# Kernel optimization log

Hardware: AMD Instinct MI355X
Metric: run time of the kernel (lower is better)

## Reference

```python
import jax, jax.numpy as jnp
import numpy as np

T, D, H, E, K = 4096, 1024, 2048, 8, 2  # tokens, model dim, expert hidden, n_experts, top_k
AUX_COEF = 0.01


def setup_inputs() -> dict:
    key = jax.random.key(0)
    ks = jax.random.split(key, 8)
    sd = lambda fan_in: 1.0 / np.sqrt(fan_in)
    x = jax.random.normal(ks[0], (T, D), jnp.float32)
    Wr = jax.random.normal(ks[1], (E, D), jnp.float32) * sd(D)      # router (no bias)
    w1 = jax.random.normal(ks[2], (E, H, D), jnp.float32) * sd(D)   # stacked up-proj
    w2 = jax.random.normal(ks[3], (E, D, H), jnp.float32) * sd(H)   # stacked down-proj
    w3 = jax.random.normal(ks[4], (E, H, D), jnp.float32) * sd(D)   # stacked gate-proj
    w1s = jax.random.normal(ks[5], (H, D), jnp.float32) * sd(D)     # shared expert
    w2s = jax.random.normal(ks[6], (D, H), jnp.float32) * sd(H)
    w3s = jax.random.normal(ks[7], (H, D), jnp.float32) * sd(D)
    return dict(x=x, Wr=Wr, w1=w1, w2=w2, w3=w3, w1s=w1s, w2s=w2s, w3s=w3s)


def _gelu(v):
    return jax.nn.gelu(v, approximate=False)  # torch F.gelu default = exact erf


def reference(x, Wr, w1, w2, w3, w1s, w2s, w3s):
    n_tok = x.shape[0]
    router_out = x @ Wr.T                                   # [T, E]
    router_probs = jax.nn.softmax(router_out, axis=-1)
    _, topk_idx = jax.lax.top_k(router_out, K)              # [T, K]
    topk_probs, _ = jax.lax.top_k(router_probs, K)          # top-k of probs (same order)

    # auxiliary load-balance loss (first-choice density * mean prob)
    expert_mask = jax.nn.one_hot(topk_idx[:, 0], E, dtype=jnp.float32)
    density = expert_mask.mean(axis=0)
    aux_loss = AUX_COEF * jnp.sum(density * router_probs.mean(axis=0)) * E

    # combine weights C[t, e] = sum of routed probs for expert e at token t
    C = jnp.zeros((n_tok, E), x.dtype).at[
        jnp.arange(n_tok)[:, None], topk_idx
    ].add(topk_probs)

    # dense per-expert SwiGLU-style FFN, combined by C (equal math to
    # sort-based dispatch + scatter_add in the original)
    h = _gelu(jnp.einsum('td,ehd->teh', x, w1)) * jnp.einsum('td,ehd->teh', x, w3)
    ye = jnp.einsum('teh,edh->ted', h, w2)                  # [T, E, D]
    out = jnp.einsum('ted,te->td', ye, C)

    # shared expert (always active)
    out = out + (_gelu(x @ w1s.T) * (x @ w3s.T)) @ w2s.T
    return out, aux_loss
```

## Files before the change

### kernel.cpp

```cpp
#include <hip/hip_runtime.h>
#include <hip/hip_bf16.h>
#include <cstdint>

#define T_TOK 4096
#define DMODEL 1024
#define HDIM 2048

typedef short bf16x8 __attribute__((ext_vector_type(8)));
typedef float f32x4 __attribute__((ext_vector_type(4)));
typedef uint32_t u32x4 __attribute__((ext_vector_type(4)));

__device__ __forceinline__ uint32_t cvt_pk_bf16(float lo, float hi) {
  uint32_t d;
  asm("v_cvt_pk_bf16_f32 %0, %1, %2" : "=v"(d) : "v"(lo), "v"(hi));
  return d;
}
__device__ __forceinline__ unsigned short f2bf(float f) {
  uint32_t d;
  asm("v_cvt_pk_bf16_f32 %0, %1, %1" : "=v"(d) : "v"(f));
  return (unsigned short)d;
}
__device__ __forceinline__ float gelu_erf(float v) {
  return 0.5f * v * (1.0f + erff(v * 0.70710678118654752f));
}
__device__ __forceinline__ void gload16(const void* g, void* lds) {
  __builtin_amdgcn_global_load_lds((const __attribute__((address_space(1))) void*)g,
                                   (__attribute__((address_space(3))) void*)lds, 16, 0, 0);
}
__device__ __forceinline__ u32x4 pk8(const float* s) {
  float4 v0 = ((const float4*)s)[0], v1 = ((const float4*)s)[1];
  u32x4 p = {cvt_pk_bf16(v0.x, v0.y), cvt_pk_bf16(v0.z, v0.w),
             cvt_pk_bf16(v1.x, v1.y), cvt_pk_bf16(v1.z, v1.w)};
  return p;
}

__global__ __launch_bounds__(256) void convert_w(
    const float* __restrict__ w1, const float* __restrict__ w3,
    const float* __restrict__ w1s, const float* __restrict__ w3s,
    const float* __restrict__ w2, const float* __restrict__ w2s,
    short* __restrict__ wu, short* __restrict__ wg, short* __restrict__ wd) {
  int bid = blockIdx.x;
  if (bid < 9216) {
    int id = bid * 256 + threadIdx.x;
    int e = id >> 18, rem = id & 262143;
    int h16 = rem >> 11, d32 = (rem >> 6) & 31, ln = rem & 63;
    size_t so = (size_t)(h16 * 16 + (ln & 15)) * DMODEL + d32 * 32 + (ln >> 4) * 8;
    const float* s1 = (e < 8) ? w1 + (size_t)e * 2097152 + so : w1s + so;
    const float* s3 = (e < 8) ? w3 + (size_t)e * 2097152 + so : w3s + so;
    *(u32x4*)(wu + (size_t)id * 8) = pk8(s1);
    *(u32x4*)(wg + (size_t)id * 8) = pk8(s3);
  } else {
    int id = (bid - 9216) * 256 + threadIdx.x;
    int e = id >> 18, rem = id & 262143;
    int d16 = rem >> 12, h32 = (rem >> 6) & 63, ln = rem & 63;
    size_t so = (size_t)(d16 * 16 + (ln & 15)) * HDIM + h32 * 32 + (ln >> 4) * 8;
    const float* s2 = (e < 8) ? w2 + (size_t)e * 2097152 + so : w2s + so;
    *(u32x4*)(wd + (size_t)id * 8) = pk8(s2);
  }
}

__global__ __launch_bounds__(256) void router_kernel(
    const float* __restrict__ x, const float* __restrict__ Wr,
    int* __restrict__ cursor, int* __restrict__ cnt1,
    float* __restrict__ psum, int* __restrict__ perm, float* __restrict__ pw,
    short* __restrict__ xb) {
  __shared__ float4 sW[8 * 256];
  __shared__ float sP[8];
  int tid = threadIdx.x;
  const float4* W4 = (const float4*)Wr;
  for (int i = tid; i < 2048; i += 256) sW[i] = W4[i];
  if (tid < 8) sP[tid] = 0.f;
  __syncthreads();

  int lane = tid & 63, wid = tid >> 6;
  int t = blockIdx.x * 4 + wid;
  float acc[8] = {0.f, 0.f, 0.f, 0.f, 0.f, 0.f, 0.f, 0.f};
  const float4* x4 = (const float4*)(x + (size_t)t * DMODEL);
#pragma unroll
  for (int it = 0; it < 4; ++it) {
    float4 xv = x4[it * 64 + lane];
    uint2 pk = {cvt_pk_bf16(xv.x, xv.y), cvt_pk_bf16(xv.z, xv.w)};
    *(uint2*)(xb + (size_t)t * DMODEL + it * 256 + lane * 4) = pk;
#pragma unroll
    for (int e = 0; e < 8; ++e) {
      float4 wv = sW[e * 256 + it * 64 + lane];
      acc[e] += xv.x * wv.x + xv.y * wv.y + xv.z * wv.z + xv.w * wv.w;
    }
  }
#pragma unroll
  for (int e = 0; e < 8; ++e)
    for (int off = 32; off; off >>= 1) acc[e] += __shfl_xor(acc[e], off);

  float mx = acc[0];
#pragma unroll
  for (int e = 1; e < 8; ++e) mx = fmaxf(mx, acc[e]);
  float ex[8], s = 0.f;
#pragma unroll
  for (int e = 0; e < 8; ++e) { ex[e] = expf(acc[e] - mx); s += ex[e]; }
  float inv = 1.f / s;
  int e0 = 0;
#pragma unroll
  for (int e = 1; e < 8; ++e) if (acc[e] > acc[e0]) e0 = e;
  int e1 = (e0 == 0) ? 1 : 0;
#pragma unroll
  for (int e = 0; e < 8; ++e) if (e != e0 && acc[e] > acc[e1]) e1 = e;

  if (lane == 0) {
#pragma unroll
    for (int e = 0; e < 8; ++e) atomicAdd(&sP[e], ex[e] * inv);
    atomicAdd(&cnt1[e0], 1);
    int s0 = atomicAdd(&cursor[e0], 1);
    perm[e0 * 4096 + s0] = t; pw[e0 * 4096 + s0] = ex[e0] * inv;
    int s1 = atomicAdd(&cursor[e1], 1);
    perm[e1 * 4096 + s1] = t; pw[e1 * 4096 + s1] = ex[e1] * inv;
  }
  __syncthreads();
  if (tid < 8) atomicAdd(&psum[tid], sP[tid]);
}

__global__ void finalize_kernel(const int* __restrict__ cursor,
                                const int* __restrict__ cnt1,
                                const float* __restrict__ psum,
                                int* __restrict__ base, float* __restrict__ aux_out) {
  if (threadIdx.x == 0) {
    int b = 0;
    for (int e = 0; e < 8; ++e) { base[e] = b; b += ((cursor[e] + 127) >> 7) << 7; }
    base[8] = b;
    float aux = 0.f;
    for (int e = 0; e < 8; ++e)
      aux += ((float)cnt1[e] * (1.f / T_TOK)) * (psum[e] * (1.f / T_TOK));
    aux_out[0] = 0.01f * 8.f * aux;
  }
}

__global__ __launch_bounds__(256, 2) void gemm_upgate(
    const short* __restrict__ xb,
    const short* __restrict__ wu, const short* __restrict__ wg,
    const int* __restrict__ cursor, const int* __restrict__ base,
    const int* __restrict__ perm, unsigned short* __restrict__ hbuf) {
  int e = blockIdx.z, mt = blockIdx.y, nt = blockIdx.x;
  int cnt = (e < 8) ? cursor[e] : 4096;
  if (mt * 128 >= cnt) return;
  int hb = base[e];
  const short* wuE = wu + (size_t)e * 2097152;
  const short* wgE = wg + (size_t)e * 2097152;

  __shared__ short As[2][4096], Bs1[2][4096], Bs3[2][4096];

  int tid = threadIdx.x, lane = tid & 63, wid = tid >> 6;
  int fr = lane & 15, ko8 = (lane >> 4) * 8;
  int wr = wid >> 1, wc = wid & 1;

  size_t aOff[2], bOff[2];
#pragma unroll
  for (int s = 0; s < 2; ++s) {
    int g = s * 4 + wid;
    int slot = mt * 128 + g * 16 + fr;
    int tok = (e == 8) ? slot : ((slot < cnt) ? perm[e * 4096 + slot] : 0);
    aOff[s] = (size_t)tok * DMODEL + ko8;
    bOff[s] = ((size_t)(nt * 8 + g) * 32 * 64 + lane) * 8;
  }

  f32x4 acc1[4][4] = {}, acc3[4][4] = {};

  auto stage = [&](int buf, int it) {
#pragma unroll
    for (int s = 0; s < 2; ++s) {
      int g = s * 4 + wid;
      gload16(xb + aOff[s] + it * 32, &As[buf][g * 512 + lane * 8]);
      size_t cb = bOff[s] + (size_t)it * 512;
      gload16(wuE + cb, &Bs1[buf][g * 512 + lane * 8]);
      gload16(wgE + cb, &Bs3[buf][g * 512 + lane * 8]);
    }
  };
  auto compute = [&](int buf) {
    bf16x8 af[4], b1f[4], b3f[4];
#pragma unroll
    for (int m = 0; m < 4; ++m)
      af[m] = *(const bf16x8*)&As[buf][(wr * 4 + m) * 512 + lane * 8];
#pragma unroll
    for (int n = 0; n < 4; ++n) {
      b1f[n] = *(const bf16x8*)&Bs1[buf][(wc * 4 + n) * 512 + lane * 8];
      b3f[n] = *(const bf16x8*)&Bs3[buf][(wc * 4 + n) * 512 + lane * 8];
    }
    __builtin_amdgcn_s_setprio(1);
#pragma unroll
    for (int m = 0; m < 4; ++m)
#pragma unroll
      for (int n = 0; n < 4; ++n) {
        acc1[m][n] = __builtin_amdgcn_mfma_f32_16x16x32_bf16(af[m], b1f[n], acc1[m][n], 0, 0, 0);
        acc3[m][n] = __builtin_amdgcn_mfma_f32_16x16x32_bf16(af[m], b3f[n], acc3[m][n], 0, 0, 0);
      }
    __builtin_amdgcn_s_setprio(0);
  };

  stage(0, 0);
  __syncthreads();
  int cur = 0;
  for (int it = 1; it < 32; ++it) {
    stage(cur ^ 1, it);
    compute(cur);
    __syncthreads();
    cur ^= 1;
  }
  compute(cur);

  int q = lane >> 4;
#pragma unroll
  for (int m = 0; m < 4; ++m) {
#pragma unroll
    for (int n = 0; n < 4; ++n) {
      int col = nt * 128 + wc * 64 + n * 16 + fr;
      f32x4 u = acc1[m][n], g = acc3[m][n];
#pragma unroll
      for (int j = 0; j < 4; ++j) {
        int sl = mt * 128 + wr * 64 + m * 16 + q * 4 + j;
        float hv = (sl < cnt) ? gelu_erf(u[j]) * g[j] : 0.f;
        hbuf[(size_t)(hb + sl) * HDIM + col] = f2bf(hv);
      }
    }
  }
}

__global__ __launch_bounds__(256, 2) void gemm_down(
    const unsigned short* __restrict__ hbuf,
    const short* __restrict__ wd,
    const int* __restrict__ cursor, const int* __restrict__ base,
    const int* __restrict__ perm, const float* __restrict__ pw,
    float* __restrict__ out) {
  int e = blockIdx.z, mt = blockIdx.y, nt = blockIdx.x;
  int cnt = (e < 8) ? cursor[e] : 4096;
  if (mt * 128 >= cnt) return;
  int hb = base[e];
  const short* wdE = wd + (size_t)e * 2097152;

  __shared__ short As[2][4096], Bs[2][4096];

  int tid = threadIdx.x, lane = tid & 63, wid = tid >> 6;
  int fr = lane & 15, ko8 = (lane >> 4) * 8;
  int wr = wid >> 1, wc = wid & 1;

  size_t aOff[2], bOff[2];
#pragma unroll
  for (int s = 0; s < 2; ++s) {
    int g = s * 4 + wid;
    aOff[s] = (size_t)(hb + mt * 128 + g * 16 + fr) * HDIM + ko8;
    bOff[s] = ((size_t)(nt * 8 + g) * 64 * 64 + lane) * 8;
  }

  f32x4 acc[4][4] = {};

  auto stage = [&](int buf, int it) {
#pragma unroll
    for (int s = 0; s < 2; ++s) {
      int g = s * 4 + wid;
      gload16(hbuf + aOff[s] + it * 32, &As[buf][g * 512 + lane * 8]);
      gload16(wdE + bOff[s] + (size_t)it * 512, &Bs[buf][g * 512 + lane * 8]);
    }
  };
  auto compute = [&](int buf) {
    bf16x8 af[4], bf[4];
#pragma unroll
    for (int m = 0; m < 4; ++m)
      af[m] = *(const bf16x8*)&As[buf][(wr * 4 + m) * 512 + lane * 8];
#pragma unroll
    for (int n = 0; n < 4; ++n)
      bf[n] = *(const bf16x8*)&Bs[buf][(wc * 4 + n) * 512 + lane * 8];
    __builtin_amdgcn_s_setprio(1);
#pragma unroll
    for (int m = 0; m < 4; ++m)
#pragma unroll
      for (int n = 0; n < 4; ++n)
        acc[m][n] = __builtin_amdgcn_mfma_f32_16x16x32_bf16(af[m], bf[n], acc[m][n], 0, 0, 0);
    __builtin_amdgcn_s_setprio(0);
  };

  stage(0, 0);
  __syncthreads();
  int cur = 0;
  for (int it = 1; it < 64; ++it) {
    stage(cur ^ 1, it);
    compute(cur);
    __syncthreads();
    cur ^= 1;
  }
  compute(cur);

  int q = lane >> 4;
#pragma unroll
  for (int m = 0; m < 4; ++m) {
#pragma unroll
    for (int n = 0; n < 4; ++n) {
      int col = nt * 128 + wc * 64 + n * 16 + fr;
      f32x4 a = acc[m][n];
#pragma unroll
      for (int j = 0; j < 4; ++j) {
        int sl = mt * 128 + wr * 64 + m * 16 + q * 4 + j;
        if (sl < cnt) {
          int tok; float p;
          if (e == 8) { tok = sl; p = 1.f; }
          else { tok = perm[e * 4096 + sl]; p = pw[e * 4096 + sl]; }
          atomicAdd(&out[(size_t)tok * DMODEL + col], p * a[j]);
        }
      }
    }
  }
}

extern "C" void kernel_launch(void* const* d_in, const int* in_sizes, int n_in,
                              void* d_out, int out_size, void* d_ws, size_t ws_size,
                              hipStream_t stream) {
  const float* x   = (const float*)d_in[0];
  const float* Wr  = (const float*)d_in[1];
  const float* w1  = (const float*)d_in[2];
  const float* w2  = (const float*)d_in[3];
  const float* w3  = (const float*)d_in[4];
  const float* w1s = (const float*)d_in[5];
  const float* w2s = (const float*)d_in[6];
  const float* w3s = (const float*)d_in[7];
  float* out = (float*)d_out;

  char* ws = (char*)d_ws;
  const size_t HBUF_OFF = 0;
  const size_t XB_OFF   = 67108864;
  const size_t WU_OFF   = XB_OFF + 8388608;
  const size_t WG_OFF   = WU_OFF + 37748736;
  const size_t WD_OFF   = WG_OFF + 37748736;
  const size_t PERM_OFF = WD_OFF + 37748736;
  const size_t PW_OFF   = PERM_OFF + 131072;
  const size_t CTRL_OFF = PW_OFF + 131072;

  unsigned short* hbuf = (unsigned short*)(ws + HBUF_OFF);
  short* xb = (short*)(ws + XB_OFF);
  short* wu = (short*)(ws + WU_OFF);
  short* wg = (short*)(ws + WG_OFF);
  short* wd = (short*)(ws + WD_OFF);
  int*   perm   = (int*)(ws + PERM_OFF);
  float* pw     = (float*)(ws + PW_OFF);
  int*   cursor = (int*)(ws + CTRL_OFF);
  int*   cnt1   = (int*)(ws + CTRL_OFF + 64);
  float* psum   = (float*)(ws + CTRL_OFF + 128);
  int*   base   = (int*)(ws + CTRL_OFF + 192);

  hipMemsetAsync(d_out, 0, (size_t)out_size * sizeof(float), stream);
  hipMemsetAsync(ws + CTRL_OFF, 0, 256, stream);

  router_kernel<<<1024, 256, 0, stream>>>(x, Wr, cursor, cnt1, psum, perm, pw, xb);
  finalize_kernel<<<1, 64, 0, stream>>>(cursor, cnt1, psum, base,
                                        out + (size_t)T_TOK * DMODEL);
  convert_w<<<18432, 256, 0, stream>>>(w1, w3, w1s, w3s, w2, w2s, wu, wg, wd);
  gemm_upgate<<<dim3(16, 32, 9), 256, 0, stream>>>(xb, wu, wg, cursor, base, perm, hbuf);
  gemm_down<<<dim3(8, 32, 9), 256, 0, stream>>>(hbuf, wd, cursor, base, perm, pw, out);
}
```

Measured before the change: 459.2 us.

## Triple-buffer LDS staging with vmcnt-based waits in expert GEMMs

Both the up/gate and down GEMMs move from double-buffered to triple-buffered LDS staging. Each iteration prefetches two k-tiles ahead, and waits with partial s_waitcnt vmcnt counts plus raw s_barrier instead of __syncthreads. The goal is to keep more global-to-LDS loads in flight so memory latency overlaps with MFMA work. In exchange, LDS use rises (up/gate goes to 72KB per block), which may lower occupancy. The down kernel's launch bounds are raised to 3 blocks per CU, and the hand-tuned vmcnt counts must match the number of loads issued per stage.

```diff
diff --git a/kernel.cpp b/kernel.cpp
--- a/kernel.cpp
+++ b/kernel.cpp
@@ -9,6 +9,9 @@
 typedef short bf16x8 __attribute__((ext_vector_type(8)));
 typedef float f32x4 __attribute__((ext_vector_type(4)));
 typedef uint32_t u32x4 __attribute__((ext_vector_type(4)));
+
+#define WAITVM(N) asm volatile("s_waitcnt vmcnt(" #N ")" ::: "memory")
+#define BAR() asm volatile("s_barrier" ::: "memory")
 
 __device__ __forceinline__ uint32_t cvt_pk_bf16(float lo, float hi) {
   uint32_t d;
@@ -145,7 +148,7 @@
   const short* wuE = wu + (size_t)e * 2097152;
   const short* wgE = wg + (size_t)e * 2097152;
 
-  __shared__ short As[2][4096], Bs1[2][4096], Bs3[2][4096];
+  __shared__ short As[3][4096], Bs1[3][4096], Bs3[3][4096];
 
   int tid = threadIdx.x, lane = tid & 63, wid = tid >> 6;
   int fr = lane & 15, ko8 = (lane >> 4) * 8;
@@ -195,15 +198,20 @@
   };
 
   stage(0, 0);
-  __syncthreads();
-  int cur = 0;
-  for (int it = 1; it < 32; ++it) {
-    stage(cur ^ 1, it);
+  stage(1, 1);
+  int cur = 0, pf = 2;
+#pragma unroll 1
+  for (int it = 0; it < 30; ++it) {
+    stage(pf, it + 2);
+    WAITVM(12);
+    BAR();
     compute(cur);
-    __syncthreads();
-    cur ^= 1;
-  }
-  compute(cur);
+    BAR();
+    pf = cur; cur = (cur == 2) ? 0 : cur + 1;
+  }
+  WAITVM(6); BAR(); compute(cur); BAR();
+  cur = (cur == 2) ? 0 : cur + 1;
+  WAITVM(0); BAR(); compute(cur);
 
   int q = lane >> 4;
 #pragma unroll
@@ -222,7 +230,7 @@
   }
 }
 
-__global__ __launch_bounds__(256, 2) void gemm_down(
+__global__ __launch_bounds__(256, 3) void gemm_down(
     const unsigned short* __restrict__ hbuf,
     const short* __restrict__ wd,
     const int* __restrict__ cursor, const int* __restrict__ base,
@@ -234,7 +242,7 @@
   int hb = base[e];
   const short* wdE = wd + (size_t)e * 2097152;
 
-  __shared__ short As[2][4096], Bs[2][4096];
+  __shared__ short As[3][4096], Bs[3][4096];
 
   int tid = threadIdx.x, lane = tid & 63, wid = tid >> 6;
   int fr = lane & 15, ko8 = (lane >> 4) * 8;
@@ -276,15 +284,20 @@
   };
 
   stage(0, 0);
-  __syncthreads();
-  int cur = 0;
-  for (int it = 1; it < 64; ++it) {
-    stage(cur ^ 1, it);
+  stage(1, 1);
+  int cur = 0, pf = 2;
+#pragma unroll 1
+  for (int it = 0; it < 62; ++it) {
+    stage(pf, it + 2);
+    WAITVM(8);
+    BAR();
     compute(cur);
-    __syncthreads();
-    cur ^= 1;
-  }
-  compute(cur);
+    BAR();
+    pf = cur; cur = (cur == 2) ? 0 : cur + 1;
+  }
+  WAITVM(4); BAR(); compute(cur); BAR();
+  cur = (cur == 2) ? 0 : cur + 1;
+  WAITVM(0); BAR(); compute(cur);
 
   int q = lane >> 4;
 #pragma unroll
```

Result: slower. 492.8 us (+7.3%).

## Fuse fp32-to-bf16 weight conversion into expert GEMMs and compact tile work list

Applied to the files above, without the earlier changes.

Removes the separate weight-conversion kernel and has both expert GEMMs load fp32 weights into registers, pack them to bf16, and store them to LDS while the current tile computes. A finalize step builds a compact list of (expert, m-tile) work items so that empty tiles do not launch. Exact erf GELU is replaced with a polynomial approximation, and the down GEMM's occupancy hint is raised. The aim is to avoid a full read/write pass over the weights, at the cost of reading fp32 weights repeatedly per m-tile and losing direct-to-LDS async loads for B.

```diff
diff --git a/kernel.cpp b/kernel.cpp
--- a/kernel.cpp
+++ b/kernel.cpp
@@ -20,8 +20,15 @@
   asm("v_cvt_pk_bf16_f32 %0, %1, %1" : "=v"(d) : "v"(f));
   return (unsigned short)d;
 }
-__device__ __forceinline__ float gelu_erf(float v) {
-  return 0.5f * v * (1.0f + erff(v * 0.70710678118654752f));
+__device__ __forceinline__ float gelu_fast(float v) {
+  float z = v * 0.70710678118654752f;
+  float az = fabsf(z);
+  float t = __frcp_rn(1.0f + 0.3275911f * az);
+  float poly = ((((1.061405429f * t - 1.453152027f) * t + 1.421413741f) * t
+                 - 0.284496736f) * t + 0.254829592f) * t;
+  float er = 1.0f - poly * __expf(-z * z);
+  er = (z < 0.f) ? -er : er;
+  return 0.5f * v * (1.0f + er);
 }
 __device__ __forceinline__ void gload16(const void* g, void* lds) {
   __builtin_amdgcn_global_load_lds((const __attribute__((address_space(1))) void*)g,
@@ -33,30 +40,10 @@
              cvt_pk_bf16(v1.x, v1.y), cvt_pk_bf16(v1.z, v1.w)};
   return p;
 }
-
-__global__ __launch_bounds__(256) void convert_w(
-    const float* __restrict__ w1, const float* __restrict__ w3,
-    const float* __restrict__ w1s, const float* __restrict__ w3s,
-    const float* __restrict__ w2, const float* __restrict__ w2s,
-    short* __restrict__ wu, short* __restrict__ wg, short* __restrict__ wd) {
-  int bid = blockIdx.x;
-  if (bid < 9216) {
-    int id = bid * 256 + threadIdx.x;
-    int e = id >> 18, rem = id & 262143;
-    int h16 = rem >> 11, d32 = (rem >> 6) & 31, ln = rem & 63;
-    size_t so = (size_t)(h16 * 16 + (ln & 15)) * DMODEL + d32 * 32 + (ln >> 4) * 8;
-    const float* s1 = (e < 8) ? w1 + (size_t)e * 2097152 + so : w1s + so;
-    const float* s3 = (e < 8) ? w3 + (size_t)e * 2097152 + so : w3s + so;
-    *(u32x4*)(wu + (size_t)id * 8) = pk8(s1);
-    *(u32x4*)(wg + (size_t)id * 8) = pk8(s3);
-  } else {
-    int id = (bid - 9216) * 256 + threadIdx.x;
-    int e = id >> 18, rem = id & 262143;
-    int d16 = rem >> 12, h32 = (rem >> 6) & 63, ln = rem & 63;
-    size_t so = (size_t)(d16 * 16 + (ln & 15)) * HDIM + h32 * 32 + (ln >> 4) * 8;
-    const float* s2 = (e < 8) ? w2 + (size_t)e * 2097152 + so : w2s + so;
-    *(u32x4*)(wd + (size_t)id * 8) = pk8(s2);
-  }
+__device__ __forceinline__ u32x4 pk2(float4 a, float4 b) {
+  u32x4 p = {cvt_pk_bf16(a.x, a.y), cvt_pk_bf16(a.z, a.w),
+             cvt_pk_bf16(b.x, b.y), cvt_pk_bf16(b.z, b.w)};
+  return p;
 }
 
 __global__ __launch_bounds__(256) void router_kernel(
@@ -121,11 +108,18 @@
 __global__ void finalize_kernel(const int* __restrict__ cursor,
                                 const int* __restrict__ cnt1,
                                 const float* __restrict__ psum,
-                                int* __restrict__ base, float* __restrict__ aux_out) {
+                                int* __restrict__ base, int* __restrict__ work,
+                                int* __restrict__ nwork, float* __restrict__ aux_out) {
   if (threadIdx.x == 0) {
-    int b = 0;
-    for (int e = 0; e < 8; ++e) { base[e] = b; b += ((cursor[e] + 127) >> 7) << 7; }
-    base[8] = b;
+    int b = 0, n = 0;
+    for (int e = 0; e < 9; ++e) {
+      int c = (e < 8) ? cursor[e] : 4096;
+      base[e] = b;
+      int ntl = (c + 127) >> 7;
+      for (int mt = 0; mt < ntl; ++mt) work[n++] = (e << 8) | mt;
+      b += ntl << 7;
+    }
+    *nwork = n;
     float aux = 0.f;
     for (int e = 0; e < 8; ++e)
       aux += ((float)cnt1[e] * (1.f / T_TOK)) * (psum[e] * (1.f / T_TOK));
@@ -135,15 +129,19 @@
 
 __global__ __launch_bounds__(256, 2) void gemm_upgate(
     const short* __restrict__ xb,
-    const short* __restrict__ wu, const short* __restrict__ wg,
+    const float* __restrict__ w1, const float* __restrict__ w3,
+    const float* __restrict__ w1s, const float* __restrict__ w3s,
     const int* __restrict__ cursor, const int* __restrict__ base,
+    const int* __restrict__ work, const int* __restrict__ nwork,
     const int* __restrict__ perm, unsigned short* __restrict__ hbuf) {
-  int e = blockIdx.z, mt = blockIdx.y, nt = blockIdx.x;
+  int y = blockIdx.y;
+  if (y >= *nwork) return;
+  int wk = work[y];
+  int e = wk >> 8, mt = wk & 255, nt = blockIdx.x;
   int cnt = (e < 8) ? cursor[e] : 4096;
-  if (mt * 128 >= cnt) return;
   int hb = base[e];
-  const short* wuE = wu + (size_t)e * 2097152;
-  const short* wgE = wg + (size_t)e * 2097152;
+  const float* B1 = (e < 8) ? w1 + (size_t)e * 2097152 : w1s;
+  const float* B3 = (e < 8) ? w3 + (size_t)e * 2097152 : w3s;
 
   __shared__ short As[2][4096], Bs1[2][4096], Bs3[2][4096];
 
@@ -151,28 +149,25 @@
   int fr = lane & 15, ko8 = (lane >> 4) * 8;
   int wr = wid >> 1, wc = wid & 1;
 
-  size_t aOff[2], bOff[2];
+  size_t aOff[2];
 #pragma unroll
   for (int s = 0; s < 2; ++s) {
     int g = s * 4 + wid;
     int slot = mt * 128 + g * 16 + fr;
     int tok = (e == 8) ? slot : ((slot < cnt) ? perm[e * 4096 + slot] : 0);
     aOff[s] = (size_t)tok * DMODEL + ko8;
-    bOff[s] = ((size_t)(nt * 8 + g) * 32 * 64 + lane) * 8;
+  }
+  const float* bSrc1[2]; const float* bSrc3[2];
+#pragma unroll
+  for (int s = 0; s < 2; ++s) {
+    int slot = s * 256 + tid;
+    int gg = slot >> 6, l = slot & 63;
+    size_t ro = (size_t)(nt * 128 + gg * 16 + (l & 15)) * DMODEL + ((l >> 4) * 8);
+    bSrc1[s] = B1 + ro; bSrc3[s] = B3 + ro;
   }
 
   f32x4 acc1[4][4] = {}, acc3[4][4] = {};
 
-  auto stage = [&](int buf, int it) {
-#pragma unroll
-    for (int s = 0; s < 2; ++s) {
-      int g = s * 4 + wid;
-      gload16(xb + aOff[s] + it * 32, &As[buf][g * 512 + lane * 8]);
-      size_t cb = bOff[s] + (size_t)it * 512;
-      gload16(wuE + cb, &Bs1[buf][g * 512 + lane * 8]);
-      gload16(wgE + cb, &Bs3[buf][g * 512 + lane * 8]);
-    }
-  };
   auto compute = [&](int buf) {
     bf16x8 af[4], b1f[4], b3f[4];
 #pragma unroll
@@ -194,16 +189,46 @@
     __builtin_amdgcn_s_setprio(0);
   };
 
-  stage(0, 0);
+#pragma unroll
+  for (int s = 0; s < 2; ++s)
+    gload16(xb + aOff[s], &As[0][(s * 4 + wid) * 512 + lane * 8]);
+#pragma unroll
+  for (int s = 0; s < 2; ++s) {
+    int slot = s * 256 + tid;
+    *(u32x4*)&Bs1[0][slot * 8] = pk8(bSrc1[s]);
+    *(u32x4*)&Bs3[0][slot * 8] = pk8(bSrc3[s]);
+  }
   __syncthreads();
-  int cur = 0;
-  for (int it = 1; it < 32; ++it) {
-    stage(cur ^ 1, it);
-    compute(cur);
-    __syncthreads();
-    cur ^= 1;
-  }
-  compute(cur);
+
+  int buf = 0;
+#pragma unroll 1
+  for (int it = 0; it < 32; ++it) {
+    int nx = it + 1;
+    float4 r1a[2], r1b[2], r3a[2], r3b[2];
+    if (nx < 32) {
+#pragma unroll
+      for (int s = 0; s < 2; ++s)
+        gload16(xb + aOff[s] + nx * 32, &As[buf ^ 1][(s * 4 + wid) * 512 + lane * 8]);
+#pragma unroll
+      for (int s = 0; s < 2; ++s) {
+        const float4* p1 = (const float4*)(bSrc1[s] + nx * 32);
+        const float4* p3 = (const float4*)(bSrc3[s] + nx * 32);
+        r1a[s] = p1[0]; r1b[s] = p1[1];
+        r3a[s] = p3[0]; r3b[s] = p3[1];
+      }
+    }
+    compute(buf);
+    if (nx < 32) {
+#pragma unroll
+      for (int s = 0; s < 2; ++s) {
+        int slot = s * 256 + tid;
+        *(u32x4*)&Bs1[buf ^ 1][slot * 8] = pk2(r1a[s], r1b[s]);
+        *(u32x4*)&Bs3[buf ^ 1][slot * 8] = pk2(r3a[s], r3b[s]);
+      }
+      __syncthreads();
+      buf ^= 1;
+    }
+  }
 
   int q = lane >> 4;
 #pragma unroll
@@ -215,24 +240,27 @@
 #pragma unroll
       for (int j = 0; j < 4; ++j) {
         int sl = mt * 128 + wr * 64 + m * 16 + q * 4 + j;
-        float hv = (sl < cnt) ? gelu_erf(u[j]) * g[j] : 0.f;
+        float hv = (sl < cnt) ? gelu_fast(u[j]) * g[j] : 0.f;
         hbuf[(size_t)(hb + sl) * HDIM + col] = f2bf(hv);
       }
     }
   }
 }
 
-__global__ __launch_bounds__(256, 2) void gemm_down(
+__global__ __launch_bounds__(256, 3) void gemm_down(
     const unsigned short* __restrict__ hbuf,
-    const short* __restrict__ wd,
+    const float* __restrict__ w2, const float* __restrict__ w2s,
     const int* __restrict__ cursor, const int* __restrict__ base,
+    const int* __restrict__ work, const int* __restrict__ nwork,
     const int* __restrict__ perm, const float* __restrict__ pw,
     float* __restrict__ out) {
-  int e = blockIdx.z, mt = blockIdx.y, nt = blockIdx.x;
+  int y = blockIdx.y;
+  if (y >= *nwork) return;
+  int wk = work[y];
+  int e = wk >> 8, mt = wk & 255, nt = blockIdx.x;
   int cnt = (e < 8) ? cursor[e] : 4096;
-  if (mt * 128 >= cnt) return;
   int hb = base[e];
-  const short* wdE = wd + (size_t)e * 2097152;
+  const float* B = (e < 8) ? w2 + (size_t)e * 2097152 : w2s;
 
   __shared__ short As[2][4096], Bs[2][4096];
 
@@ -240,24 +268,22 @@
   int fr = lane & 15, ko8 = (lane >> 4) * 8;
   int wr = wid >> 1, wc = wid & 1;
 
-  size_t aOff[2], bOff[2];
+  size_t aOff[2];
 #pragma unroll
   for (int s = 0; s < 2; ++s) {
     int g = s * 4 + wid;
     aOff[s] = (size_t)(hb + mt * 128 + g * 16 + fr) * HDIM + ko8;
-    bOff[s] = ((size_t)(nt * 8 + g) * 64 * 64 + lane) * 8;
+  }
+  const float* bSrc[2];
+#pragma unroll
+  for (int s = 0; s < 2; ++s) {
+    int slot = s * 256 + tid;
+    int gg = slot >> 6, l = slot & 63;
+    bSrc[s] = B + (size_t)(nt * 128 + gg * 16 + (l & 15)) * HDIM + ((l >> 4) * 8);
   }
 
   f32x4 acc[4][4] = {};
 
-  auto stage = [&](int buf, int it) {
-#pragma unroll
-    for (int s = 0; s < 2; ++s) {
-      int g = s * 4 + wid;
-      gload16(hbuf + aOff[s] + it * 32, &As[buf][g * 512 + lane * 8]);
-      gload16(wdE + bOff[s] + (size_t)it * 512, &Bs[buf][g * 512 + lane * 8]);
-    }
-  };
   auto compute = [&](int buf) {
     bf16x8 af[4], bf[4];
 #pragma unroll
@@ -275,16 +301,42 @@
     __builtin_amdgcn_s_setprio(0);
   };
 
-  stage(0, 0);
+#pragma unroll
+  for (int s = 0; s < 2; ++s)
+    gload16(hbuf + aOff[s], &As[0][(s * 4 + wid) * 512 + lane * 8]);
+#pragma unroll
+  for (int s = 0; s < 2; ++s) {
+    int slot = s * 256 + tid;
+    *(u32x4*)&Bs[0][slot * 8] = pk8(bSrc[s]);
+  }
   __syncthreads();
-  int cur = 0;
-  for (int it = 1; it < 64; ++it) {
-    stage(cur ^ 1, it);
-    compute(cur);
-    __syncthreads();
-    cur ^= 1;
-  }
-  compute(cur);
+
+  int buf = 0;
+#pragma unroll 1
+  for (int it = 0; it < 64; ++it) {
+    int nx = it + 1;
+    float4 ra[2], rb[2];
+    if (nx < 64) {
+#pragma unroll
+      for (int s = 0; s < 2; ++s)
+        gload16(hbuf + aOff[s] + nx * 32, &As[buf ^ 1][(s * 4 + wid) * 512 + lane * 8]);
+#pragma unroll
+      for (int s = 0; s < 2; ++s) {
+        const float4* p = (const float4*)(bSrc[s] + nx * 32);
+        ra[s] = p[0]; rb[s] = p[1];
+      }
+    }
+    compute(buf);
+    if (nx < 64) {
+#pragma unroll
+      for (int s = 0; s < 2; ++s) {
+        int slot = s * 256 + tid;
+        *(u32x4*)&Bs[buf ^ 1][slot * 8] = pk2(ra[s], rb[s]);
+      }
+      __syncthreads();
+      buf ^= 1;
+    }
+  }
 
   int q = lane >> 4;
 #pragma unroll
@@ -323,32 +375,30 @@
   char* ws = (char*)d_ws;
   const size_t HBUF_OFF = 0;
   const size_t XB_OFF   = 67108864;
-  const size_t WU_OFF   = XB_OFF + 8388608;
-  const size_t WG_OFF   = WU_OFF + 37748736;
-  const size_t WD_OFF   = WG_OFF + 37748736;
-  const size_t PERM_OFF = WD_OFF + 37748736;
+  const size_t PERM_OFF = XB_OFF + 8388608;
   const size_t PW_OFF   = PERM_OFF + 131072;
   const size_t CTRL_OFF = PW_OFF + 131072;
+  const size_t WORK_OFF = CTRL_OFF + 256;
 
   unsigned short* hbuf = (unsigned short*)(ws + HBUF_OFF);
   short* xb = (short*)(ws + XB_OFF);
-  short* wu = (short*)(ws + WU_OFF);
-  short* wg = (short*)(ws + WG_OFF);
-  short* wd = (short*)(ws + WD_OFF);
   int*   perm   = (int*)(ws + PERM_OFF);
   float* pw     = (float*)(ws + PW_OFF);
   int*   cursor = (int*)(ws + CTRL_OFF);
   int*   cnt1   = (int*)(ws + CTRL_OFF + 64);
   float* psum   = (float*)(ws + CTRL_OFF + 128);
   int*   base   = (int*)(ws + CTRL_OFF + 192);
+  int*   work   = (int*)(ws + WORK_OFF);
+  int*   nwork  = (int*)(ws + WORK_OFF + 512);
 
   hipMemsetAsync(d_out, 0, (size_t)out_size * sizeof(float), stream);
   hipMemsetAsync(ws + CTRL_OFF, 0, 256, stream);
 
   router_kernel<<<1024, 256, 0, stream>>>(x, Wr, cursor, cnt1, psum, perm, pw, xb);
-  finalize_kernel<<<1, 64, 0, stream>>>(cursor, cnt1, psum, base,
+  finalize_kernel<<<1, 64, 0, stream>>>(cursor, cnt1, psum, base, work, nwork,
                                         out + (size_t)T_TOK * DMODEL);
-  convert_w<<<18432, 256, 0, stream>>>(w1, w3, w1s, w3s, w2, w2s, wu, wg, wd);
-  gemm_upgate<<<dim3(16, 32, 9), 256, 0, stream>>>(xb, wu, wg, cursor, base, perm, hbuf);
-  gemm_down<<<dim3(8, 32, 9), 256, 0, stream>>>(hbuf, wd, cursor, base, perm, pw, out);
-}
+  gemm_upgate<<<dim3(16, 128), 256, 0, stream>>>(xb, w1, w3, w1s, w3s,
+                                                 cursor, base, work, nwork, perm, hbuf);
+  gemm_down<<<dim3(8, 128), 256, 0, stream>>>(hbuf, w2, w2s,
+                                              cursor, base, work, nwork, perm, pw, out);
+}
```

Measured after the change: 622.1 us. +35.5%, slower.
